# Performance work log

Measured on AMD Instinct MI355X. Metric: run time of the kernel, lower is better.

Reference implementation:

```python
import jax, jax.numpy as jnp
import numpy as np


def setup_inputs() -> dict:
    key = jax.random.key(0)
    k1, k2, k3, k4 = jax.random.split(key, 4)
    B, C, H, W = 2, 3, 160, 160
    n, L, s, k = 3000, 72, 4, 5
    return {
        "x": jax.random.normal(k1, (B, C, H, W), dtype=jnp.float32),
        "queries": jax.random.normal(k2, (B, L, H, W), dtype=jnp.float32),
        "keys": jax.random.normal(k3, (n, L), dtype=jnp.float32),
        "values": jax.random.normal(k4, (n, s * s, k * k), dtype=jnp.float32),
        "s": s,
        "k": k,
    }


def reference(x, queries, keys, values, s, k):
    B, C, H, W = x.shape
    pad = k // 2
    # reflect-pad spatial dims (matches F.pad mode='reflect')
    xp = jnp.pad(x, ((0, 0), (0, 0), (pad, pad), (pad, pad)), mode="reflect")
    # extract k*k patches: [B, C, H, W, k*k] (fixed small loop over k*k offsets)
    patches = jnp.stack(
        [xp[:, :, i : i + H, j : j + W] for i in range(k) for j in range(k)],
        axis=-1,
    )
    # per-pixel top-1 routing over codebook keys
    q = queries.transpose(0, 2, 3, 1)  # [B, H, W, L]
    sim = jnp.einsum("bhwl,nl->bhwn", q, keys)  # [B, H, W, n]
    idx = jnp.argmax(sim, axis=-1)  # [B, H, W] int
    v = values[idx]  # gather per-pixel kernel: [B, H, W, s^2, k^2]
    # per-pixel dynamic conv: [B, C, s^2, H, W]
    out = jnp.einsum("bchwk,bhwsk->bcshw", patches, v)
    # pixel shuffle with upscale s: [B, C, s^2, H, W] -> [B, C, H*s, W*s]
    out = out.reshape(B, C, s, s, H, W)
    out = out.transpose(0, 1, 4, 2, 5, 3)  # [B, C, H, s, W, s]
    return out.reshape(B, C, H * s, W * s)
```

## Files before the change

### kernel.cpp

```cpp
#include <hip/hip_runtime.h>

#define H 160
#define W 160
#define HW 25600
#define BB 2
#define CC 3
#define LL 72
#define NKEYS 3000
#define NT 94
#define NSPL 4
#define NPIX (BB * HW)

#define CERR 3e-5f
#define ABSG 1e-3f

typedef __attribute__((ext_vector_type(8))) short bf8v;
typedef __attribute__((ext_vector_type(16))) float f16v;

union FU { uint4 u4; bf8v v; };

#define WS_KFRAG 1024
#define WS_B1    963584
#define WS_B2    1782784
#define WS_BI    2601984
#define WS_THR   3421184
#define WS_LIST  3625984
#define WS_IDX   3830784

#define GPTR(p) ((const __attribute__((address_space(1))) void*)(p))
#define LPTR(p) ((__attribute__((address_space(3))) void*)(p))

__device__ inline unsigned bf16rn(float f) {
    unsigned u = __float_as_uint(f);
    return (u + 0x7FFFu + ((u >> 16) & 1u)) >> 16;
}

__global__ __launch_bounds__(64) void kprep_kernel(
    const float* __restrict__ keys, unsigned* __restrict__ ctrl,
    uint4* __restrict__ kfg)
{
    const int tile = blockIdx.x;
    const int lane = threadIdx.x;
    const int key  = tile * 32 + (lane & 31);
    const int half = lane >> 5;
    const bool kv  = (key < NKEYS);
    float kmax = 0.f;
#pragma unroll
    for (int ks = 0; ks < 5; ++ks) {
        unsigned wh[4], wl[4];
#pragma unroll
        for (int j = 0; j < 4; ++j) {
            const int l0 = ks * 16 + half * 8 + 2 * j;
            float v0 = (kv && l0     < LL) ? keys[(size_t)key * LL + l0]     : 0.f;
            float v1 = (kv && l0 + 1 < LL) ? keys[(size_t)key * LL + l0 + 1] : 0.f;
            kmax = fmaxf(kmax, fmaxf(fabsf(v0), fabsf(v1)));
            unsigned h0 = bf16rn(v0), h1 = bf16rn(v1);
            float r0 = v0 - __uint_as_float(h0 << 16);
            float r1 = v1 - __uint_as_float(h1 << 16);
            wh[j] = h0 | (h1 << 16);
            wl[j] = bf16rn(r0) | (bf16rn(r1) << 16);
        }
        const int base = tile * 640 + (ks * 2) * 64 + lane;
        kfg[base]      = make_uint4(wh[0], wh[1], wh[2], wh[3]);
        kfg[base + 64] = make_uint4(wl[0], wl[1], wl[2], wl[3]);
    }
#pragma unroll
    for (int m = 32; m >= 1; m >>= 1)
        kmax = fmaxf(kmax, __shfl_xor(kmax, m));
    if (lane == 0) atomicMax(&ctrl[1], __float_as_uint(kmax));
}

__device__ __forceinline__ void build_qfrag(
    const float* __restrict__ qp, int hv, FU* qh, FU* ql, float& Ssum)
{
    Ssum = 0.f;
#pragma unroll
    for (int ks = 0; ks < 5; ++ks) {
        unsigned wh[4], wl[4];
#pragma unroll
        for (int j = 0; j < 4; ++j) {
            const int l0 = ks * 16 + hv * 8 + 2 * j;
            float v0 = (l0     < LL) ? qp[(size_t)l0 * HW]       : 0.f;
            float v1 = (l0 + 1 < LL) ? qp[(size_t)(l0 + 1) * HW] : 0.f;
            Ssum += fabsf(v0) + fabsf(v1);
            unsigned h0 = bf16rn(v0), h1 = bf16rn(v1);
            float r0 = v0 - __uint_as_float(h0 << 16);
            float r1 = v1 - __uint_as_float(h1 << 16);
            wh[j] = h0 | (h1 << 16);
            wl[j] = bf16rn(r0) | (bf16rn(r1) << 16);
        }
        qh[ks].u4 = make_uint4(wh[0], wh[1], wh[2], wh[3]);
        ql[ks].u4 = make_uint4(wl[0], wl[1], wl[2], wl[3]);
    }
}

__device__ __forceinline__ void stage_tile(
    const uint4* __restrict__ src, uint4* lbuf, int tid, int wid)
{
    __builtin_amdgcn_global_load_lds(GPTR(src + tid),
                                     LPTR(lbuf + (tid & ~63)), 16, 0, 0);
    __builtin_amdgcn_global_load_lds(GPTR(src + 256 + tid),
                                     LPTR(lbuf + 256 + (tid & ~63)), 16, 0, 0);
    if (wid < 2) {
        __builtin_amdgcn_global_load_lds(GPTR(src + 512 + tid),
                                         LPTR(lbuf + 512 + (tid & ~63)), 16, 0, 0);
    }
}

template<bool LAST>
__device__ __forceinline__ void comp_tile_lds(
    const uint4* __restrict__ kb, int tileIdx,
    const FU* __restrict__ qhA, const FU* __restrict__ qlA,
    const FU* __restrict__ qhB, const FU* __restrict__ qlB,
    int lane, int hb,
    float& b1A, float& b2A, int& biA,
    float& b1B, float& b2B, int& biB)
{
    f16v accA, accB;
#pragma unroll
    for (int r = 0; r < 16; ++r) { accA[r] = 0.f; accB[r] = 0.f; }
#pragma unroll
    for (int ks = 0; ks < 5; ++ks) {
        FU kh, kl;
        kh.u4 = kb[ks * 128 + lane];
        kl.u4 = kb[ks * 128 + 64 + lane];
        accA = __builtin_amdgcn_mfma_f32_32x32x16_bf16(kh.v, qhA[ks].v, accA, 0, 0, 0);
        accB = __builtin_amdgcn_mfma_f32_32x32x16_bf16(kh.v, qhB[ks].v, accB, 0, 0, 0);
        accA = __builtin_amdgcn_mfma_f32_32x32x16_bf16(kh.v, qlA[ks].v, accA, 0, 0, 0);
        accB = __builtin_amdgcn_mfma_f32_32x32x16_bf16(kh.v, qlB[ks].v, accB, 0, 0, 0);
        accA = __builtin_amdgcn_mfma_f32_32x32x16_bf16(kl.v, qhA[ks].v, accA, 0, 0, 0);
        accB = __builtin_amdgcn_mfma_f32_32x32x16_bf16(kl.v, qhB[ks].v, accB, 0, 0, 0);
    }
    const int kb0 = tileIdx * 32 + hb;
    const int NR = LAST ? 12 : 16;
#pragma unroll
    for (int r = 0; r < NR; ++r) {
        const int key = kb0 + ((r & 3) + 8 * (r >> 2));
        {
            const float s = accA[r];
            const float n2 = __builtin_amdgcn_fmed3f(b1A, b2A, s);
            const bool gt = (s > b1A);
            b1A = fmaxf(b1A, s); b2A = n2; biA = gt ? key : biA;
        }
        {
            const float s = accB[r];
            const float n2 = __builtin_amdgcn_fmed3f(b1B, b2B, s);
            const bool gt = (s > b1B);
            b1B = fmaxf(b1B, s); b2B = n2; biB = gt ? key : biB;
        }
    }
}

__global__ __launch_bounds__(256) void route_kernel(
    const float* __restrict__ queries,
    const uint4* __restrict__ kfg,
    const unsigned* __restrict__ ctrl,
    float* __restrict__ b1s, float* __restrict__ b2s,
    int* __restrict__ bis, float* __restrict__ thr)
{
    __shared__ uint4 sbuf[2][640];

    const int tid   = threadIdx.x;
    const int lane  = tid & 63;
    const int wid   = tid >> 6;
    const int hv    = lane >> 5;
    const int hb    = 4 * hv;
    const int split = blockIdx.y;
    const int pA = blockIdx.x * 256 + wid * 64 + (lane & 31);
    const int pB = pA + 32;

    FU qhA[5], qlA[5], qhB[5], qlB[5];
    float SsA, SsB;
    {
        const int bA = pA / HW, hwA = pA - bA * HW;
        build_qfrag(queries + (size_t)bA * LL * HW + hwA, hv, qhA, qlA, SsA);
        const int bB = pB / HW, hwB = pB - bB * HW;
        build_qfrag(queries + (size_t)bB * LL * HW + hwB, hv, qhB, qlB, SsB);
    }

    float b1A = -3.0e38f, b2A = -3.0e38f; int biA = 0;
    float b1B = -3.0e38f, b2B = -3.0e38f; int biB = 0;

    const int t0     = split * 24;
    const int tcount = (split == NSPL - 1) ? (NT - 3 * 24) : 24;

    stage_tile(kfg + (size_t)t0 * 640, sbuf[0], tid, wid);
    __syncthreads();

#pragma unroll 1
    for (int i = 0; i < tcount; i += 2) {
        stage_tile(kfg + (size_t)(t0 + i + 1) * 640, sbuf[1], tid, wid);
        comp_tile_lds<false>(sbuf[0], t0 + i, qhA, qlA, qhB, qlB, lane, hb,
                             b1A, b2A, biA, b1B, b2B, biB);
        __syncthreads();

        if (i + 2 < tcount)
            stage_tile(kfg + (size_t)(t0 + i + 2) * 640, sbuf[0], tid, wid);
        if (t0 + i + 1 == NT - 1)
            comp_tile_lds<true >(sbuf[1], t0 + i + 1, qhA, qlA, qhB, qlB, lane, hb,
                                 b1A, b2A, biA, b1B, b2B, biB);
        else
            comp_tile_lds<false>(sbuf[1], t0 + i + 1, qhA, qlA, qhB, qlB, lane, hb,
                                 b1A, b2A, biA, b1B, b2B, biB);
        __syncthreads();
    }

    const float o1A = __shfl_xor(b1A, 32), o2A = __shfl_xor(b2A, 32);
    const int   oiA = __shfl_xor(biA, 32);
    const float n2A = fmaxf(fminf(b1A, o1A), fmaxf(b2A, o2A));
    const bool  tkA = (o1A > b1A) || (o1A == b1A && oiA < biA);
    const float n1A = fmaxf(b1A, o1A);
    const int   niA = tkA ? oiA : biA;

    const float o1B = __shfl_xor(b1B, 32), o2B = __shfl_xor(b2B, 32);
    const int   oiB = __shfl_xor(biB, 32);
    const float n2B = fmaxf(fminf(b1B, o1B), fmaxf(b2B, o2B));
    const bool  tkB = (o1B > b1B) || (o1B == b1B && oiB < biB);
    const float n1B = fmaxf(b1B, o1B);
    const int   niB = tkB ? oiB : biB;

    if ((lane & 32) == 0) {
        const int sp = split * NPIX;
        b1s[sp + pA] = n1A; b2s[sp + pA] = n2A; bis[sp + pA] = niA;
        b1s[sp + pB] = n1B; b2s[sp + pB] = n2B; bis[sp + pB] = niB;
        if (split == 0) {
            const float kmax = __uint_as_float(ctrl[1]);
            const float SpA = SsA + __shfl_xor(SsA, 32);
            const float SpB = SsB + __shfl_xor(SsB, 32);
            thr[pA] = 2.0f * (CERR * SpA * kmax + ABSG);
            thr[pB] = 2.0f * (CERR * SpB * kmax + ABSG);
        }
    }
}

__global__ __launch_bounds__(256) void combine_kernel(
    const float* __restrict__ b1s, const float* __restrict__ b2s,
    const int* __restrict__ bis, const float* __restrict__ thr,
    unsigned* __restrict__ ctrl, unsigned* __restrict__ list,
    int* __restrict__ idx_buf)
{
    const int p = blockIdx.x * 256 + threadIdx.x;
    float m1 = -3.0e38f, m2 = -3.0e38f; int bi = 0;
#pragma unroll
    for (int s = 0; s < NSPL; ++s) {
        const float a1 = b1s[s * NPIX + p];
        const float a2 = b2s[s * NPIX + p];
        const int   ai = bis[s * NPIX + p];
        if (a1 > m1) { m2 = fmaxf(m1, a2); m1 = a1; bi = ai; }
        else         { m2 = fmaxf(m2, a1); }
    }
    if ((m1 - m2) > thr[p]) idx_buf[p] = bi;
    else { unsigned pos = atomicAdd(&ctrl[0], 1u); list[pos] = (unsigned)p; }
}

__global__ __launch_bounds__(256) void cleanup_kernel(
    const float* __restrict__ queries, const float* __restrict__ keys,
    const unsigned* __restrict__ ctrl, const unsigned* __restrict__ list,
    int* __restrict__ idx_buf)
{
    __shared__ float qs[LL];
    __shared__ float rbest[4];
    __shared__ int   ridx[4];

    const int tid = threadIdx.x;
    const int ln  = tid & 63;
    const int wid = tid >> 6;
    const unsigned count = ctrl[0];

    for (unsigned u = blockIdx.x; u < count; u += gridDim.x) {
        const int p  = (int)list[u];
        const int b  = p / HW;
        const int hw = p - b * HW;

        __syncthreads();
        if (tid < LL)
            qs[tid] = queries[((size_t)b * LL + tid) * HW + hw];
        __syncthreads();

        float q[LL];
#pragma unroll
        for (int l = 0; l < LL; ++l) q[l] = qs[l];

        float best = -3.0e38f; int bidx = 0x7FFFFFFF;
#pragma unroll 1
        for (int it = 0; it < 12; ++it) {
            const int n  = it * 256 + tid;
            const int nc = (n < NKEYS) ? n : (NKEYS - 1);
            const float4* __restrict__ kr = (const float4*)(keys + (size_t)nc * LL);
            float a0 = 0.f, a1 = 0.f, a2 = 0.f, a3 = 0.f;
#pragma unroll
            for (int j = 0; j < 18; ++j) {
                float4 kv = kr[j];
                a0 = fmaf(q[4 * j + 0], kv.x, a0);
                a1 = fmaf(q[4 * j + 1], kv.y, a1);
                a2 = fmaf(q[4 * j + 2], kv.z, a2);
                a3 = fmaf(q[4 * j + 3], kv.w, a3);
            }
            const float s = (a0 + a1) + (a2 + a3);
            if (n < NKEYS && (s > best || (s == best && n < bidx))) { best = s; bidx = n; }
        }
#pragma unroll
        for (int m = 32; m >= 1; m >>= 1) {
            const float ob = __shfl_xor(best, m);
            const int   oi = __shfl_xor(bidx, m);
            if (ob > best || (ob == best && oi < bidx)) { best = ob; bidx = oi; }
        }
        if (ln == 0) { rbest[wid] = best; ridx[wid] = bidx; }
        __syncthreads();
        if (tid == 0) {
            float fb = rbest[0]; int fi = ridx[0];
#pragma unroll
            for (int wvi = 1; wvi < 4; ++wvi) {
                if (rbest[wvi] > fb || (rbest[wvi] == fb && ridx[wvi] < fi)) {
                    fb = rbest[wvi]; fi = ridx[wvi];
                }
            }
            idx_buf[p] = fi;
        }
    }
}

__global__ __launch_bounds__(256) void conv_kernel(
    const float* __restrict__ x,
    const float* __restrict__ values,
    const int* __restrict__ idx_buf,
    float* __restrict__ out)
{
    const int p  = blockIdx.x * 256 + threadIdx.x;
    const int b  = p / HW;
    const int hw = p - b * HW;
    const int h  = hw / W;
    const int w  = hw - h * W;

    const int idx = idx_buf[p];

    float patch[CC][25];
#pragma unroll
    for (int i = 0; i < 5; ++i) {
        int r = h + i - 2;
        r = (r < 0) ? -r : ((r >= H) ? (2 * H - 2 - r) : r);
#pragma unroll
        for (int j = 0; j < 5; ++j) {
            int cidx = w + j - 2;
            cidx = (cidx < 0) ? -cidx : ((cidx >= W) ? (2 * W - 2 - cidx) : cidx);
#pragma unroll
            for (int c = 0; c < CC; ++c)
                patch[c][i * 5 + j] = x[((size_t)(b * CC + c) * H + r) * W + cidx];
        }
    }

    const float* vbase = values + (size_t)idx * 400;
    float acc[CC][16];
#pragma unroll
    for (int c = 0; c < CC; ++c)
#pragma unroll
        for (int si = 0; si < 16; ++si) acc[c][si] = 0.f;

#pragma unroll
    for (int si = 0; si < 16; ++si) {
        float v[25];
#pragma unroll
        for (int kk = 0; kk < 25; ++kk) v[kk] = vbase[si * 25 + kk];
#pragma unroll
        for (int c = 0; c < CC; ++c) {
            float a = 0.f;
#pragma unroll
            for (int kk = 0; kk < 25; ++kk) a += patch[c][kk] * v[kk];
            acc[c][si] = a;
        }
    }

#pragma unroll
    for (int c = 0; c < CC; ++c) {
#pragma unroll
        for (int sy = 0; sy < 4; ++sy) {
            float4 o = make_float4(acc[c][sy * 4 + 0], acc[c][sy * 4 + 1],
                                   acc[c][sy * 4 + 2], acc[c][sy * 4 + 3]);
            size_t off = ((size_t)(b * CC + c) * (H * 4) + (h * 4 + sy)) * (size_t)(W * 4)
                         + (size_t)w * 4;
            *(float4*)(&out[off]) = o;
        }
    }
}

extern "C" void kernel_launch(void* const* d_in, const int* in_sizes, int n_in,
                              void* d_out, int out_size, void* d_ws, size_t ws_size,
                              hipStream_t stream) {
    const float* x       = (const float*)d_in[0];
    const float* queries = (const float*)d_in[1];
    const float* keys    = (const float*)d_in[2];
    const float* values  = (const float*)d_in[3];
    float* out = (float*)d_out;

    char* ws = (char*)d_ws;
    unsigned* ctrl = (unsigned*)ws;
    uint4*    kfg  = (uint4*)(ws + WS_KFRAG);
    float*    b1s  = (float*)(ws + WS_B1);
    float*    b2s  = (float*)(ws + WS_B2);
    int*      bis  = (int*)(ws + WS_BI);
    float*    thr  = (float*)(ws + WS_THR);
    unsigned* list = (unsigned*)(ws + WS_LIST);
    int*      idxb = (int*)(ws + WS_IDX);

    hipMemsetAsync(d_ws, 0, 8, stream);
    kprep_kernel<<<NT, 64, 0, stream>>>(keys, ctrl, kfg);
    route_kernel<<<dim3(NPIX / 256, NSPL), 256, 0, stream>>>(queries, kfg, ctrl,
                                                             b1s, b2s, bis, thr);
    combine_kernel<<<NPIX / 256, 256, 0, stream>>>(b1s, b2s, bis, thr, ctrl, list, idxb);
    cleanup_kernel<<<2048, 256, 0, stream>>>(queries, keys, ctrl, list, idxb);
    conv_kernel<<<NPIX / 256, 256, 0, stream>>>(x, values, idxb, out);
}
```

Measured before the change: 174.9 us.

## Triple-buffer key tiles with explicit vmcnt waits and early prefetch

Replaces the double-buffered per-tile staging in the routing kernel with a three-slot ring that loads two key tiles per stage. Waits use explicit s_waitcnt vmcnt counts and raw s_barrier instead of __syncthreads, and the first two stages are issued before the query fragments are built, so key loads overlap query preparation. The aim is to hide global-to-LDS latency and cut the number of barriers. In exchange LDS use grows from 20 KB to 60 KB per block, which may lower occupancy, and the hand-counted vmcnt values must match the loads actually in flight or the kernel reads stale data.

```diff
diff --git a/kernel.cpp b/kernel.cpp
--- a/kernel.cpp
+++ b/kernel.cpp
@@ -30,6 +30,10 @@
 #define GPTR(p) ((const __attribute__((address_space(1))) void*)(p))
 #define LPTR(p) ((__attribute__((address_space(3))) void*)(p))
 
+#define BARRIER() do { asm volatile("" ::: "memory"); \
+                       __builtin_amdgcn_s_barrier();  \
+                       asm volatile("" ::: "memory"); } while (0)
+
 __device__ inline unsigned bf16rn(float f) {
     unsigned u = __float_as_uint(f);
     return (u + 0x7FFFu + ((u >> 16) & 1u)) >> 16;
@@ -94,19 +98,6 @@
     }
 }
 
-__device__ __forceinline__ void stage_tile(
-    const uint4* __restrict__ src, uint4* lbuf, int tid, int wid)
-{
-    __builtin_amdgcn_global_load_lds(GPTR(src + tid),
-                                     LPTR(lbuf + (tid & ~63)), 16, 0, 0);
-    __builtin_amdgcn_global_load_lds(GPTR(src + 256 + tid),
-                                     LPTR(lbuf + 256 + (tid & ~63)), 16, 0, 0);
-    if (wid < 2) {
-        __builtin_amdgcn_global_load_lds(GPTR(src + 512 + tid),
-                                         LPTR(lbuf + 512 + (tid & ~63)), 16, 0, 0);
-    }
-}
-
 template<bool LAST>
 __device__ __forceinline__ void comp_tile_lds(
     const uint4* __restrict__ kb, int tileIdx,
@@ -151,60 +142,13 @@
     }
 }
 
-__global__ __launch_bounds__(256) void route_kernel(
-    const float* __restrict__ queries,
-    const uint4* __restrict__ kfg,
+__device__ __forceinline__ void merge_store(
+    float b1A, float b2A, int biA, float b1B, float b2B, int biB,
+    float SsA, float SsB, int lane, int split, int pA, int pB,
     const unsigned* __restrict__ ctrl,
     float* __restrict__ b1s, float* __restrict__ b2s,
     int* __restrict__ bis, float* __restrict__ thr)
 {
-    __shared__ uint4 sbuf[2][640];
-
-    const int tid   = threadIdx.x;
-    const int lane  = tid & 63;
-    const int wid   = tid >> 6;
-    const int hv    = lane >> 5;
-    const int hb    = 4 * hv;
-    const int split = blockIdx.y;
-    const int pA = blockIdx.x * 256 + wid * 64 + (lane & 31);
-    const int pB = pA + 32;
-
-    FU qhA[5], qlA[5], qhB[5], qlB[5];
-    float SsA, SsB;
-    {
-        const int bA = pA / HW, hwA = pA - bA * HW;
-        build_qfrag(queries + (size_t)bA * LL * HW + hwA, hv, qhA, qlA, SsA);
-        const int bB = pB / HW, hwB = pB - bB * HW;
-        build_qfrag(queries + (size_t)bB * LL * HW + hwB, hv, qhB, qlB, SsB);
-    }
-
-    float b1A = -3.0e38f, b2A = -3.0e38f; int biA = 0;
-    float b1B = -3.0e38f, b2B = -3.0e38f; int biB = 0;
-
-    const int t0     = split * 24;
-    const int tcount = (split == NSPL - 1) ? (NT - 3 * 24) : 24;
-
-    stage_tile(kfg + (size_t)t0 * 640, sbuf[0], tid, wid);
-    __syncthreads();
-
-#pragma unroll 1
-    for (int i = 0; i < tcount; i += 2) {
-        stage_tile(kfg + (size_t)(t0 + i + 1) * 640, sbuf[1], tid, wid);
-        comp_tile_lds<false>(sbuf[0], t0 + i, qhA, qlA, qhB, qlB, lane, hb,
-                             b1A, b2A, biA, b1B, b2B, biB);
-        __syncthreads();
-
-        if (i + 2 < tcount)
-            stage_tile(kfg + (size_t)(t0 + i + 2) * 640, sbuf[0], tid, wid);
-        if (t0 + i + 1 == NT - 1)
-            comp_tile_lds<true >(sbuf[1], t0 + i + 1, qhA, qlA, qhB, qlB, lane, hb,
-                                 b1A, b2A, biA, b1B, b2B, biB);
-        else
-            comp_tile_lds<false>(sbuf[1], t0 + i + 1, qhA, qlA, qhB, qlB, lane, hb,
-                                 b1A, b2A, biA, b1B, b2B, biB);
-        __syncthreads();
-    }
-
     const float o1A = __shfl_xor(b1A, 32), o2A = __shfl_xor(b2A, 32);
     const int   oiA = __shfl_xor(biA, 32);
     const float n2A = fmaxf(fminf(b1A, o1A), fmaxf(b2A, o2A));
@@ -233,6 +177,77 @@
     }
 }
 
+__device__ __forceinline__ void stage_pair_async(
+    const uint4* __restrict__ src, uint4* lbuf, int tid)
+{
+#pragma unroll
+    for (int j = 0; j < 5; ++j)
+        __builtin_amdgcn_global_load_lds(GPTR(src + j * 256 + tid),
+                                         LPTR(lbuf + j * 256 + (tid & ~63)), 16, 0, 0);
+}
+
+__global__ __launch_bounds__(256) void route_kernel(
+    const float* __restrict__ queries,
+    const uint4* __restrict__ kfg,
+    const unsigned* __restrict__ ctrl,
+    float* __restrict__ b1s, float* __restrict__ b2s,
+    int* __restrict__ bis, float* __restrict__ thr)
+{
+    __shared__ uint4 sbuf[3 * 1280];
+
+    const int tid   = threadIdx.x;
+    const int lane  = tid & 63;
+    const int wid   = tid >> 6;
+    const int hv    = lane >> 5;
+    const int hb    = 4 * hv;
+    const int split = blockIdx.y;
+    const int pA = blockIdx.x * 256 + wid * 64 + (lane & 31);
+    const int pB = pA + 32;
+
+    const uint4* __restrict__ kbase = kfg + (size_t)split * 24 * 640;
+    const int t0    = split * 24;
+    const int npair = (split == NSPL - 1) ? 11 : 12;
+
+    stage_pair_async(kbase, sbuf, tid);
+    stage_pair_async(kbase + 1280, sbuf + 1280, tid);
+
+    FU qhA[5], qlA[5], qhB[5], qlB[5];
+    float SsA, SsB;
+    {
+        const int bA = pA / HW, hwA = pA - bA * HW;
+        build_qfrag(queries + (size_t)bA * LL * HW + hwA, hv, qhA, qlA, SsA);
+        const int bB = pB / HW, hwB = pB - bB * HW;
+        build_qfrag(queries + (size_t)bB * LL * HW + hwB, hv, qhB, qlB, SsB);
+    }
+
+    float b1A = -3.0e38f, b2A = -3.0e38f; int biA = 0;
+    float b1B = -3.0e38f, b2B = -3.0e38f; int biB = 0;
+
+#pragma unroll 1
+    for (int g = 0; g < npair; ++g) {
+        BARRIER();
+        if (g + 2 < npair)
+            stage_pair_async(kbase + (size_t)(g + 2) * 1280,
+                             sbuf + ((g + 2) % 3) * 1280, tid);
+        if (g + 2 < npair)      asm volatile("s_waitcnt vmcnt(10)" ::: "memory");
+        else if (g + 1 < npair) asm volatile("s_waitcnt vmcnt(5)"  ::: "memory");
+        else                    asm volatile("s_waitcnt vmcnt(0)"  ::: "memory");
+        BARRIER();
+        const uint4* kb = sbuf + (g % 3) * 1280;
+        comp_tile_lds<false>(kb, t0 + 2 * g, qhA, qlA, qhB, qlB, lane, hb,
+                             b1A, b2A, biA, b1B, b2B, biB);
+        if (t0 + 2 * g + 1 == NT - 1)
+            comp_tile_lds<true >(kb + 640, t0 + 2 * g + 1, qhA, qlA, qhB, qlB,
+                                 lane, hb, b1A, b2A, biA, b1B, b2B, biB);
+        else
+            comp_tile_lds<false>(kb + 640, t0 + 2 * g + 1, qhA, qlA, qhB, qlB,
+                                 lane, hb, b1A, b2A, biA, b1B, b2B, biB);
+    }
+
+    merge_store(b1A, b2A, biA, b1B, b2B, biB, SsA, SsB, lane, split, pA, pB,
+                ctrl, b1s, b2s, bis, thr);
+}
+
 __global__ __launch_bounds__(256) void combine_kernel(
     const float* __restrict__ b1s, const float* __restrict__ b2s,
     const int* __restrict__ bis, const float* __restrict__ thr,
```

Result: faster. 169.1 us (-3.3%).
